# Kernel optimization log

Hardware: AMD Instinct MI355X
Metric: run time of the kernel (lower is better)

The kernel has to match this reference:

```python
import jax, jax.numpy as jnp
import numpy as np

N, E = 50000, 300000
IN, HID, OUT, HEADS = 768, 256, 128, 8
RELS = ("writes", "written_by", "cites")


def setup_inputs():
    ks = iter(jax.random.split(jax.random.key(0), 64))

    def nrm(shape, scale=1.0):
        return jax.random.normal(next(ks), shape, dtype=jnp.float32) * scale

    inp = {"x_paper": nrm((N, IN)), "x_author": nrm((N, IN))}
    for name in ("ei_writes", "ei_written_by", "ei_cites"):
        inp[name] = jax.random.randint(next(ks), (2, E), 0, N, dtype=jnp.int32)
    # layer 0: in=IN, out=HID, heads=HEADS
    s0 = 1.0 / np.sqrt(IN)
    inp["W0_paper"] = nrm((IN, HID), s0); inp["b0_paper"] = jnp.zeros((HID,), jnp.float32)
    inp["W0_author"] = nrm((IN, HID), s0); inp["b0_author"] = jnp.zeros((HID,), jnp.float32)
    D0 = HID // HEADS
    for rel in RELS:
        inp["a0s_" + rel] = nrm((HEADS, D0), 0.1)
        inp["a0d_" + rel] = nrm((HEADS, D0), 0.1)
    inp["Wk0"] = nrm((HID, HID), 1.0 / np.sqrt(HID)); inp["bk0"] = jnp.zeros((HID,), jnp.float32)
    inp["q0"] = nrm((HID,), 0.1)
    # layer 1 (last): in=HID, out=OUT, heads=1
    s1 = 1.0 / np.sqrt(HID)
    inp["W1_paper"] = nrm((HID, OUT), s1); inp["b1_paper"] = jnp.zeros((OUT,), jnp.float32)
    inp["W1_author"] = nrm((HID, OUT), s1); inp["b1_author"] = jnp.zeros((OUT,), jnp.float32)
    for rel in RELS:
        inp["a1s_" + rel] = nrm((1, OUT), 0.1)
        inp["a1d_" + rel] = nrm((1, OUT), 0.1)
    inp["Wk1"] = nrm((OUT, OUT), 1.0 / np.sqrt(OUT)); inp["bk1"] = jnp.zeros((OUT,), jnp.float32)
    inp["q1"] = nrm((OUT,), 0.1)
    return inp


def _han_layer(xs, proj, att, Wk, bk, q, edges, heads):
    # xs: {ntype: [N, in]}, proj: {ntype: (W, b)}, att: {rel: (a_src[H,D], a_dst[H,D])}
    C = q.shape[0]
    D = C // heads
    xh = {nt: (x @ proj[nt][0] + proj[nt][1]).reshape(-1, heads, D) for nt, x in xs.items()}
    outs = {nt: [] for nt in xs}
    for (st, rel, dt), ei in edges:
        a_s, a_d = att[rel]
        xsrc, xdst = xh[st], xh[dt]
        src, dst = ei[0], ei[1]
        n = xdst.shape[0]
        # GAT-style edge scores per head: [E, H]
        al = jax.nn.leaky_relu((xsrc * a_s).sum(-1)[src] + (xdst * a_d).sum(-1)[dst], 0.2)
        amax = jax.lax.stop_gradient(jax.ops.segment_max(al, dst, num_segments=n))
        ex = jnp.exp(al - amax[dst])
        alpha = ex / (jax.ops.segment_sum(ex, dst, num_segments=n)[dst] + 1e-16)
        msg = xsrc[src] * alpha[:, :, None]                      # [E, H, D]
        agg = jax.ops.segment_sum(msg, dst, num_segments=n)      # [n, H, D]
        outs[dt].append(jax.nn.relu(agg.reshape(n, C)))
    # semantic attention across metapaths (group)
    res = {}
    for nt, lst in outs.items():
        stk = jnp.stack(lst)                                     # [M, n, C]
        score = (q * jnp.tanh(stk @ Wk + bk).mean(axis=1)).sum(-1)
        w = jax.nn.softmax(score)                                # [M]
        res[nt] = jnp.einsum('m,mnc->nc', w, stk)
    return res


def reference(x_paper, x_author, W0_paper, b0_paper, W0_author, b0_author,
              a0s_writes, a0d_writes, a0s_written_by, a0d_written_by, a0s_cites, a0d_cites,
              Wk0, bk0, q0,
              W1_paper, b1_paper, W1_author, b1_author,
              a1s_writes, a1d_writes, a1s_written_by, a1d_written_by, a1s_cites, a1d_cites,
              Wk1, bk1, q1,
              ei_writes, ei_written_by, ei_cites):
    edges = [(("author", "writes", "paper"), ei_writes),
             (("paper", "written_by", "author"), ei_written_by),
             (("paper", "cites", "paper"), ei_cites)]
    h = _han_layer({"paper": x_paper, "author": x_author},
                   {"paper": (W0_paper, b0_paper), "author": (W0_author, b0_author)},
                   {"writes": (a0s_writes, a0d_writes),
                    "written_by": (a0s_written_by, a0d_written_by),
                    "cites": (a0s_cites, a0d_cites)},
                   Wk0, bk0, q0, edges, HEADS)
    h = {k: jax.nn.elu(v) for k, v in h.items()}
    h = _han_layer(h,
                   {"paper": (W1_paper, b1_paper), "author": (W1_author, b1_author)},
                   {"writes": (a1s_writes, a1d_writes),
                    "written_by": (a1s_written_by, a1d_written_by),
                    "cites": (a1s_cites, a1d_cites)},
                   Wk1, bk1, q1, edges, 1)

    def l2n(v):
        return v / jnp.maximum(jnp.linalg.norm(v, axis=1, keepdims=True), 1e-12)

    return (l2n(h["paper"]), l2n(h["author"]))
```

## Files before the change

### kernel.cpp

```cpp
#include <hip/hip_runtime.h>
#include <math.h>

#define NN 50000
#define NE 300000
#define DIN 768
#define DHID 256
#define DOUT 128
#define H0 8
#define D0 32

typedef __attribute__((ext_vector_type(8))) short bf16x8;
typedef __attribute__((ext_vector_type(8))) unsigned short u16x8;
typedef __attribute__((ext_vector_type(4))) float f32x4;

__device__ __forceinline__ unsigned short f2bf(float f) {
    unsigned u = __float_as_uint(f);
    unsigned r = (u + 0x7fffu + ((u >> 16) & 1u)) >> 16;
    return (unsigned short)r;
}
__device__ __forceinline__ float bf2f(unsigned short u) {
    return __uint_as_float(((unsigned)u) << 16);
}

__device__ __forceinline__ void gload16(const void* g, void* l) {
    __builtin_amdgcn_global_load_lds(
        (const __attribute__((address_space(1))) unsigned int*)g,
        (__attribute__((address_space(3))) unsigned int*)l, 16, 0, 0);
}

__global__ void convert_bf16_kernel(const float* __restrict__ in, unsigned short* __restrict__ out, int n8)
{
    int i = blockIdx.x * 256 + threadIdx.x;
    if (i >= n8) return;
    float4 a = ((const float4*)in)[i * 2];
    float4 b = ((const float4*)in)[i * 2 + 1];
    u16x8 o;
    o[0] = f2bf(a.x); o[1] = f2bf(a.y); o[2] = f2bf(a.z); o[3] = f2bf(a.w);
    o[4] = f2bf(b.x); o[5] = f2bf(b.y); o[6] = f2bf(b.z); o[7] = f2bf(b.w);
    ((u16x8*)out)[i] = o;
}

__global__ void transconv_kernel(const float* __restrict__ W, unsigned short* __restrict__ Wt,
                                 int K, int Nc)
{
    int gid = blockIdx.x * 256 + threadIdx.x;
    if (gid >= K * Nc) return;
    int k = gid / Nc, n = gid - k * Nc;
    Wt[(size_t)n * K + k] = f2bf(W[gid]);
}

__global__ __launch_bounds__(256) void gemm_bf16_kernel(
    const unsigned short* __restrict__ A0, const unsigned short* __restrict__ A1,
    const unsigned short* __restrict__ Bt0, const unsigned short* __restrict__ Bt1,
    const float* __restrict__ bias0, const float* __restrict__ bias1,
    unsigned short* __restrict__ C0, unsigned short* __restrict__ C1,
    int M, int K, int Nc)
{
    __shared__ __align__(16) unsigned short As[2][128 * 32];
    __shared__ __align__(16) unsigned short Bs[2][128 * 32];
    const int z = blockIdx.z;
    const unsigned short* A  = z ? A1  : A0;
    const unsigned short* Bt = z ? Bt1 : Bt0;
    const float* bias = z ? bias1 : bias0;
    unsigned short* C = z ? C1 : C0;
    const int t = threadIdx.x;
    const int lane = t & 63, w = t >> 6;
    const int wr = w >> 1, wc = w & 1;
    const int bm = blockIdx.y * 128, bn = blockIdx.x * 128;

    f32x4 acc[4][4];
    #pragma unroll
    for (int m = 0; m < 4; ++m)
        #pragma unroll
        for (int n = 0; n < 4; ++n)
            acc[m][n] = (f32x4){0.f, 0.f, 0.f, 0.f};

    const int c0 = w * 64 + lane, c1 = c0 + 256;
    const int row0 = c0 >> 2, row1 = c1 >> 2;
    const int g0 = (c0 & 3) ^ ((row0 >> 1) & 3);
    const int g1 = (c1 & 3) ^ ((row1 >> 1) & 3);
    const int ar0 = (bm + row0 < M) ? (bm + row0) : (M - 1);
    const int ar1 = (bm + row1 < M) ? (bm + row1) : (M - 1);
    const unsigned short* pA0 = A + (size_t)ar0 * K + g0 * 8;
    const unsigned short* pA1 = A + (size_t)ar1 * K + g1 * 8;
    const unsigned short* pB0 = Bt + (size_t)(bn + row0) * K + g0 * 8;
    const unsigned short* pB1 = Bt + (size_t)(bn + row1) * K + g1 * 8;

    const int rA = wr * 64 + (lane & 15);
    const int rB = wc * 64 + (lane & 15);
    const int gw = lane >> 4;
    const int nt = K >> 5;

    gload16(pA0, &As[0][c0 * 8]);
    gload16(pA1, &As[0][c1 * 8]);
    gload16(pB0, &Bs[0][c0 * 8]);
    gload16(pB1, &Bs[0][c1 * 8]);
    __syncthreads();
    for (int ti = 0; ti < nt; ++ti) {
        const int cur = ti & 1;
        if (ti + 1 < nt) {
            const int nk = (ti + 1) << 5;
            const int nb = cur ^ 1;
            gload16(pA0 + nk, &As[nb][c0 * 8]);
            gload16(pA1 + nk, &As[nb][c1 * 8]);
            gload16(pB0 + nk, &Bs[nb][c0 * 8]);
            gload16(pB1 + nk, &Bs[nb][c1 * 8]);
        }
        bf16x8 afr[4], bfr[4];
        #pragma unroll
        for (int m = 0; m < 4; ++m) {
            int r = rA + m * 16;
            afr[m] = *(const bf16x8*)&As[cur][r * 32 + ((gw ^ ((r >> 1) & 3)) * 8)];
        }
        #pragma unroll
        for (int n = 0; n < 4; ++n) {
            int r = rB + n * 16;
            bfr[n] = *(const bf16x8*)&Bs[cur][r * 32 + ((gw ^ ((r >> 1) & 3)) * 8)];
        }
        #pragma unroll
        for (int m = 0; m < 4; ++m)
            #pragma unroll
            for (int n = 0; n < 4; ++n)
                acc[m][n] = __builtin_amdgcn_mfma_f32_16x16x32_bf16(afr[m], bfr[n], acc[m][n], 0, 0, 0);
        __syncthreads();
    }
    #pragma unroll
    for (int m = 0; m < 4; ++m) {
        #pragma unroll
        for (int j = 0; j < 4; ++j) {
            int row = bm + wr * 64 + m * 16 + (lane >> 4) * 4 + j;
            if (row >= M) continue;
            #pragma unroll
            for (int n = 0; n < 4; ++n) {
                int col = bn + wc * 64 + n * 16 + (lane & 15);
                C[(size_t)row * Nc + col] = f2bf(acc[m][n][j] + bias[col]);
            }
        }
    }
}

__global__ __launch_bounds__(256) void sem_bf16_kernel(
    const unsigned short* __restrict__ A, const unsigned short* __restrict__ Bt,
    const float* __restrict__ bk, float* __restrict__ partial,
    int M, int K, int Nc)
{
    __shared__ __align__(16) unsigned short As[2][128 * 32];
    __shared__ __align__(16) unsigned short Bs[2][128 * 32];
    __shared__ float red[128];
    const int t = threadIdx.x;
    const int lane = t & 63, w = t >> 6;
    const int wr = w >> 1, wc = w & 1;
    const int bm = blockIdx.y * 128, bn = blockIdx.x * 128;

    f32x4 acc[4][4];
    #pragma unroll
    for (int m = 0; m < 4; ++m)
        #pragma unroll
        for (int n = 0; n < 4; ++n)
            acc[m][n] = (f32x4){0.f, 0.f, 0.f, 0.f};

    const int c0 = w * 64 + lane, c1 = c0 + 256;
    const int row0 = c0 >> 2, row1 = c1 >> 2;
    const int g0 = (c0 & 3) ^ ((row0 >> 1) & 3);
    const int g1 = (c1 & 3) ^ ((row1 >> 1) & 3);
    const int ar0 = (bm + row0 < M) ? (bm + row0) : (M - 1);
    const int ar1 = (bm + row1 < M) ? (bm + row1) : (M - 1);
    const unsigned short* pA0 = A + (size_t)ar0 * K + g0 * 8;
    const unsigned short* pA1 = A + (size_t)ar1 * K + g1 * 8;
    const unsigned short* pB0 = Bt + (size_t)(bn + row0) * K + g0 * 8;
    const unsigned short* pB1 = Bt + (size_t)(bn + row1) * K + g1 * 8;

    const int rA = wr * 64 + (lane & 15);
    const int rB = wc * 64 + (lane & 15);
    const int gw = lane >> 4;
    const int nt = K >> 5;

    gload16(pA0, &As[0][c0 * 8]);
    gload16(pA1, &As[0][c1 * 8]);
    gload16(pB0, &Bs[0][c0 * 8]);
    gload16(pB1, &Bs[0][c1 * 8]);
    __syncthreads();
    for (int ti = 0; ti < nt; ++ti) {
        const int cur = ti & 1;
        if (ti + 1 < nt) {
            const int nk = (ti + 1) << 5;
            const int nb = cur ^ 1;
            gload16(pA0 + nk, &As[nb][c0 * 8]);
            gload16(pA1 + nk, &As[nb][c1 * 8]);
            gload16(pB0 + nk, &Bs[nb][c0 * 8]);
            gload16(pB1 + nk, &Bs[nb][c1 * 8]);
        }
        bf16x8 afr[4], bfr[4];
        #pragma unroll
        for (int m = 0; m < 4; ++m) {
            int r = rA + m * 16;
            afr[m] = *(const bf16x8*)&As[cur][r * 32 + ((gw ^ ((r >> 1) & 3)) * 8)];
        }
        #pragma unroll
        for (int n = 0; n < 4; ++n) {
            int r = rB + n * 16;
            bfr[n] = *(const bf16x8*)&Bs[cur][r * 32 + ((gw ^ ((r >> 1) & 3)) * 8)];
        }
        #pragma unroll
        for (int m = 0; m < 4; ++m)
            #pragma unroll
            for (int n = 0; n < 4; ++n)
                acc[m][n] = __builtin_amdgcn_mfma_f32_16x16x32_bf16(afr[m], bfr[n], acc[m][n], 0, 0, 0);
        __syncthreads();
    }
    if (t < 128) red[t] = 0.f;
    __syncthreads();
    #pragma unroll
    for (int n = 0; n < 4; ++n) {
        int lcol = wc * 64 + n * 16 + (lane & 15);
        float b = bk[bn + lcol];
        float s = 0.f;
        #pragma unroll
        for (int m = 0; m < 4; ++m) {
            #pragma unroll
            for (int j = 0; j < 4; ++j) {
                int row = bm + wr * 64 + m * 16 + (lane >> 4) * 4 + j;
                if (row < M) s += tanhf(acc[m][n][j] + b);
            }
        }
        atomicAdd(&red[lcol], s);
    }
    __syncthreads();
    if (t < 128) atomicAdd(&partial[bn + t], red[t]);
}

__global__ void hist_kernel(const int* __restrict__ dst, int* __restrict__ deg, int E)
{
    int e = blockIdx.x * 256 + threadIdx.x;
    if (e < E) atomicAdd(&deg[dst[e]], 1);
}

__global__ void block_sum_kernel(const int* __restrict__ deg, int* __restrict__ bsum, int n)
{
    __shared__ int buf[256];
    int i = blockIdx.x * 256 + threadIdx.x;
    buf[threadIdx.x] = (i < n) ? deg[i] : 0;
    __syncthreads();
    for (int s = 128; s > 0; s >>= 1) {
        if (threadIdx.x < s) buf[threadIdx.x] += buf[threadIdx.x + s];
        __syncthreads();
    }
    if (threadIdx.x == 0) bsum[blockIdx.x] = buf[0];
}

__global__ void scan_bsum_kernel(const int* __restrict__ bsum, int* __restrict__ boff, int nb)
{
    __shared__ int buf[256];
    int tid = threadIdx.x;
    int v = (tid < nb) ? bsum[tid] : 0;
    buf[tid] = v;
    __syncthreads();
    for (int off = 1; off < 256; off <<= 1) {
        int t = (tid >= off) ? buf[tid - off] : 0;
        __syncthreads();
        buf[tid] += t;
        __syncthreads();
    }
    if (tid < nb) boff[tid] = buf[tid] - v;
}

__global__ void scan_final_kernel(const int* __restrict__ deg, const int* __restrict__ boff,
                                  int* __restrict__ offs, int n)
{
    __shared__ int buf[256];
    int tid = threadIdx.x, b = blockIdx.x;
    int i = b * 256 + tid;
    int v = (i < n) ? deg[i] : 0;
    buf[tid] = v;
    __syncthreads();
    for (int off = 1; off < 256; off <<= 1) {
        int t = (tid >= off) ? buf[tid - off] : 0;
        __syncthreads();
        buf[tid] += t;
        __syncthreads();
    }
    if (i < n) offs[i] = boff[b] + buf[tid] - v;
    if (i == n - 1) offs[n] = boff[b] + buf[tid];
}

__global__ void place_kernel(const int* __restrict__ src, const int* __restrict__ dst,
                             const int* __restrict__ offs, int* __restrict__ cnt,
                             int* __restrict__ esrc, int E)
{
    int e = blockIdx.x * 256 + threadIdx.x;
    if (e >= E) return;
    int d = dst[e];
    int p = offs[d] + atomicAdd(&cnt[d], 1);
    esrc[p] = src[e];
}

__global__ void scores_L0_kernel(
    const unsigned short* __restrict__ xp, const unsigned short* __restrict__ xa,
    const float* __restrict__ a_dw, const float* __restrict__ a_swb,
    const float* __restrict__ a_sc, const float* __restrict__ a_dc,
    const float* __restrict__ a_sw, const float* __restrict__ a_dwb,
    float* __restrict__ sW_dst, float* __restrict__ sWB_src,
    float* __restrict__ sC_src, float* __restrict__ sC_dst,
    float* __restrict__ sW_src, float* __restrict__ sWB_dst)
{
    int gid = blockIdx.x * 256 + threadIdx.x;
    int half = NN * H0;
    if (gid >= 2 * half) return;
    if (gid < half) {
        int node = gid >> 3, h = gid & 7;
        const unsigned short* xr = xp + (size_t)node * DHID + h * D0;
        float xv[D0];
        #pragma unroll
        for (int j = 0; j < 4; ++j) {
            u16x8 v = ((const u16x8*)xr)[j];
            #pragma unroll
            for (int k = 0; k < 8; ++k) xv[j * 8 + k] = bf2f(v[k]);
        }
        const float* p0 = a_dw  + h * D0;
        const float* p1 = a_swb + h * D0;
        const float* p2 = a_sc  + h * D0;
        const float* p3 = a_dc  + h * D0;
        float d0 = 0.f, d1 = 0.f, d2 = 0.f, d3 = 0.f;
        #pragma unroll
        for (int k = 0; k < D0; ++k) {
            float x = xv[k];
            d0 += x * p0[k]; d1 += x * p1[k]; d2 += x * p2[k]; d3 += x * p3[k];
        }
        sW_dst[gid] = d0; sWB_src[gid] = d1; sC_src[gid] = d2; sC_dst[gid] = d3;
    } else {
        int g = gid - half;
        int node = g >> 3, h = g & 7;
        const unsigned short* xr = xa + (size_t)node * DHID + h * D0;
        float xv[D0];
        #pragma unroll
        for (int j = 0; j < 4; ++j) {
            u16x8 v = ((const u16x8*)xr)[j];
            #pragma unroll
            for (int k = 0; k < 8; ++k) xv[j * 8 + k] = bf2f(v[k]);
        }
        const float* p0 = a_sw  + h * D0;
        const float* p1 = a_dwb + h * D0;
        float d0 = 0.f, d1 = 0.f;
        #pragma unroll
        for (int k = 0; k < D0; ++k) {
            float x = xv[k];
            d0 += x * p0[k]; d1 += x * p1[k];
        }
        sW_src[g] = d0; sWB_dst[g] = d1;
    }
}

__global__ void scores_L1_kernel(
    const unsigned short* __restrict__ xp, const unsigned short* __restrict__ xa,
    const float* __restrict__ a_dw, const float* __restrict__ a_swb,
    const float* __restrict__ a_sc, const float* __restrict__ a_dc,
    const float* __restrict__ a_sw, const float* __restrict__ a_dwb,
    float* __restrict__ sW_dst, float* __restrict__ sWB_src,
    float* __restrict__ sC_src, float* __restrict__ sC_dst,
    float* __restrict__ sW_src, float* __restrict__ sWB_dst)
{
    int gid = blockIdx.x * 256 + threadIdx.x;
    if (gid >= 2 * NN) return;
    if (gid < NN) {
        const unsigned short* xr = xp + (size_t)gid * DOUT;
        float d0 = 0.f, d1 = 0.f, d2 = 0.f, d3 = 0.f;
        for (int j = 0; j < DOUT / 8; ++j) {
            u16x8 v = ((const u16x8*)xr)[j];
            #pragma unroll
            for (int k = 0; k < 8; ++k) {
                float x = bf2f(v[k]);
                int c = j * 8 + k;
                d0 += x * a_dw[c]; d1 += x * a_swb[c]; d2 += x * a_sc[c]; d3 += x * a_dc[c];
            }
        }
        sW_dst[gid] = d0; sWB_src[gid] = d1; sC_src[gid] = d2; sC_dst[gid] = d3;
    } else {
        int g = gid - NN;
        const unsigned short* xr = xa + (size_t)g * DOUT;
        float d0 = 0.f, d1 = 0.f;
        for (int j = 0; j < DOUT / 8; ++j) {
            u16x8 v = ((const u16x8*)xr)[j];
            #pragma unroll
            for (int k = 0; k < 8; ++k) {
                float x = bf2f(v[k]);
                int c = j * 8 + k;
                d0 += x * a_sw[c]; d1 += x * a_dwb[c];
            }
        }
        sW_src[g] = d0; sWB_dst[g] = d1;
    }
}

__global__ void seg_alpha3_kernel(
    const int* __restrict__ of0, const int* __restrict__ of1, const int* __restrict__ of2,
    const int* __restrict__ es0, const int* __restrict__ es1, const int* __restrict__ es2,
    const float* __restrict__ ss0, const float* __restrict__ ss1, const float* __restrict__ ss2,
    const float* __restrict__ sd0, const float* __restrict__ sd1, const float* __restrict__ sd2,
    float* __restrict__ al0, float* __restrict__ al1, float* __restrict__ al2, int H)
{
    int rel = blockIdx.y;
    const int* offs = rel == 0 ? of0 : (rel == 1 ? of1 : of2);
    const int* esrc = rel == 0 ? es0 : (rel == 1 ? es1 : es2);
    const float* ssrc = rel == 0 ? ss0 : (rel == 1 ? ss1 : ss2);
    const float* sdst = rel == 0 ? sd0 : (rel == 1 ? sd1 : sd2);
    float* alpha = rel == 0 ? al0 : (rel == 1 ? al1 : al2);
    int gid = blockIdx.x * 256 + threadIdx.x;
    if (gid >= NN * H) return;
    int d = gid / H, h = gid - d * H;
    int beg = offs[d], end = offs[d + 1];
    float sd = sdst[gid];
    float m = -INFINITY, den = 0.f;
    for (int i = beg; i < end; ++i) {
        int s = esrc[i];
        float v = ssrc[s * H + h] + sd;
        v = (v >= 0.f) ? v : 0.2f * v;
        if (v > m) { den = den * expf(m - v) + 1.f; m = v; }
        else       den += expf(v - m);
    }
    float inv = 1.f / (den + 1e-16f);
    for (int i = beg; i < end; ++i) {
        int s = esrc[i];
        float v = ssrc[s * H + h] + sd;
        v = (v >= 0.f) ? v : 0.2f * v;
        alpha[(size_t)i * H + h] = expf(v - m) * inv;
    }
}

template<int CPL, int HH, int DSH>
__global__ __launch_bounds__(256) void gather3_kernel(
    const int* __restrict__ of0, const int* __restrict__ of1, const int* __restrict__ of2,
    const int* __restrict__ es0, const int* __restrict__ es1, const int* __restrict__ es2,
    const float* __restrict__ al0, const float* __restrict__ al1, const float* __restrict__ al2,
    const unsigned short* __restrict__ x0, const unsigned short* __restrict__ x1,
    const unsigned short* __restrict__ x2,
    unsigned short* __restrict__ o0, unsigned short* __restrict__ o1,
    unsigned short* __restrict__ o2, int C)
{
    int rel = blockIdx.y;
    const int* offs = rel == 0 ? of0 : (rel == 1 ? of1 : of2);
    const int* esrc = rel == 0 ? es0 : (rel == 1 ? es1 : es2);
    const float* alpha = rel == 0 ? al0 : (rel == 1 ? al1 : al2);
    const unsigned short* x = rel == 0 ? x0 : (rel == 1 ? x1 : x2);
    unsigned short* outp = rel == 0 ? o0 : (rel == 1 ? o1 : o2);

    int wid = threadIdx.x >> 6, lane = threadIdx.x & 63;
    int d = blockIdx.x * 4 + wid;
    int c0 = lane * CPL;
    int h = c0 >> DSH;
    int beg = offs[d], end = offs[d + 1];
    float acc[CPL];
    #pragma unroll
    for (int j = 0; j < CPL; ++j) acc[j] = 0.f;
    for (int i = beg; i < end; ++i) {
        int s = esrc[i];
        float a = alpha[(size_t)i * HH + h];
        const unsigned short* xp = x + (size_t)s * C + c0;
        if (CPL == 4) {
            ushort4 xv = *(const ushort4*)xp;
            acc[0] += a * bf2f(xv.x); acc[1] += a * bf2f(xv.y);
            acc[2] += a * bf2f(xv.z); acc[3] += a * bf2f(xv.w);
        } else {
            ushort2 xv = *(const ushort2*)xp;
            acc[0] += a * bf2f(xv.x); acc[1] += a * bf2f(xv.y);
        }
    }
    unsigned short* op = outp + (size_t)d * C + c0;
    if (CPL == 4) {
        ushort4 st;
        st.x = f2bf(fmaxf(acc[0], 0.f)); st.y = f2bf(fmaxf(acc[1], 0.f));
        st.z = f2bf(fmaxf(acc[2], 0.f)); st.w = f2bf(fmaxf(acc[3], 0.f));
        *(ushort4*)op = st;
    } else {
        ushort2 st;
        st.x = f2bf(fmaxf(acc[0], 0.f)); st.y = f2bf(fmaxf(acc[1], 0.f));
        *(ushort2*)op = st;
    }
}

__global__ void sem_weights_kernel(const float* __restrict__ partial, const float* __restrict__ q,
                                   float* __restrict__ w, int C, int n)
{
    if (threadIdx.x != 0 || blockIdx.x != 0) return;
    float inv = 1.f / (float)n;
    float s0 = 0.f, s1 = 0.f;
    for (int c = 0; c < C; ++c) {
        s0 += q[c] * partial[c] * inv;
        s1 += q[c] * partial[C + c] * inv;
    }
    float m = fmaxf(s0, s1);
    float e0 = expf(s0 - m), e1 = expf(s1 - m);
    float den = e0 + e1;
    w[0] = e0 / den;
    w[1] = e1 / den;
}

__global__ void combine2_bf16_kernel(const unsigned short* __restrict__ a,
                                     const unsigned short* __restrict__ b,
                                     const float* __restrict__ w, unsigned short* __restrict__ out,
                                     int n8)
{
    int i = blockIdx.x * 256 + threadIdx.x;
    if (i >= n8) return;
    float w0 = w[0], w1 = w[1];
    u16x8 va = ((const u16x8*)a)[i];
    u16x8 vb = ((const u16x8*)b)[i];
    u16x8 o;
    #pragma unroll
    for (int j = 0; j < 8; ++j) o[j] = f2bf(w0 * bf2f(va[j]) + w1 * bf2f(vb[j]));
    ((u16x8*)out)[i] = o;
}

__global__ __launch_bounds__(128) void final_norm_kernel(
    const unsigned short* __restrict__ aggW, const unsigned short* __restrict__ aggC,
    const unsigned short* __restrict__ aggB, const float* __restrict__ w,
    float* __restrict__ out)
{
    __shared__ float red[128];
    int row = blockIdx.x;
    int c = threadIdx.x;
    float v;
    if (row < NN) {
        size_t i = (size_t)row * DOUT + c;
        v = w[0] * bf2f(aggW[i]) + w[1] * bf2f(aggC[i]);
    } else {
        size_t i = (size_t)(row - NN) * DOUT + c;
        v = bf2f(aggB[i]);
    }
    red[c] = v * v;
    __syncthreads();
    for (int s = 64; s > 0; s >>= 1) {
        if (c < s) red[c] += red[c + s];
        __syncthreads();
    }
    float norm = sqrtf(red[0]);
    out[(size_t)row * DOUT + c] = v / fmaxf(norm, 1e-12f);
}

static void build_csr(const int* ei, int* offs, int* esrc, int* deg, int* bsum, int* boff,
                      hipStream_t stream)
{
    const int* src = ei;
    const int* dst = ei + NE;
    const int NB = (NN + 255) / 256;
    hipMemsetAsync(deg, 0, NN * sizeof(int), stream);
    hist_kernel<<<(NE + 255) / 256, 256, 0, stream>>>(dst, deg, NE);
    block_sum_kernel<<<NB, 256, 0, stream>>>(deg, bsum, NN);
    scan_bsum_kernel<<<1, 256, 0, stream>>>(bsum, boff, NB);
    scan_final_kernel<<<NB, 256, 0, stream>>>(deg, boff, offs, NN);
    hipMemsetAsync(deg, 0, NN * sizeof(int), stream);
    place_kernel<<<(NE + 255) / 256, 256, 0, stream>>>(src, dst, offs, deg, esrc, NE);
}

extern "C" void kernel_launch(void* const* d_in, const int* in_sizes, int n_in,
                              void* d_out, int out_size, void* d_ws, size_t ws_size,
                              hipStream_t stream)
{
    const float* x_paper   = (const float*)d_in[0];
    const float* x_author  = (const float*)d_in[1];
    const int*   ei_writes = (const int*)d_in[2];
    const int*   ei_wb     = (const int*)d_in[3];
    const int*   ei_cites  = (const int*)d_in[4];
    const float* W0p = (const float*)d_in[5];  const float* b0p = (const float*)d_in[6];
    const float* W0a = (const float*)d_in[7];  const float* b0a = (const float*)d_in[8];
    const float* a0s_w  = (const float*)d_in[9];  const float* a0d_w  = (const float*)d_in[10];
    const float* a0s_wb = (const float*)d_in[11]; const float* a0d_wb = (const float*)d_in[12];
    const float* a0s_c  = (const float*)d_in[13]; const float* a0d_c  = (const float*)d_in[14];
    const float* Wk0 = (const float*)d_in[15]; const float* bk0 = (const float*)d_in[16];
    const float* q0  = (const float*)d_in[17];
    const float* W1p = (const float*)d_in[18]; const float* b1p = (const float*)d_in[19];
    const float* W1a = (const float*)d_in[20]; const float* b1a = (const float*)d_in[21];
    const float* a1s_w  = (const float*)d_in[22]; const float* a1d_w  = (const float*)d_in[23];
    const float* a1s_wb = (const float*)d_in[24]; const float* a1d_wb = (const float*)d_in[25];
    const float* a1s_c  = (const float*)d_in[26]; const float* a1d_c  = (const float*)d_in[27];
    const float* Wk1 = (const float*)d_in[28]; const float* bk1 = (const float*)d_in[29];
    const float* q1  = (const float*)d_in[30];

    float* out = (float*)d_out;

    const size_t NH = (size_t)NN * DHID;
    const size_t NI = (size_t)NN * DIN;
    const size_t NO = (size_t)NN * DOUT;
    const size_t NH2 = NH * 2;
    const size_t NI2 = NI * 2;
    const size_t NO2 = NO * 2;

    char* base = (char*)d_ws;
    unsigned short* xbhP = (unsigned short*)(base + 0);
    unsigned short* xbhA = (unsigned short*)(base + NH2);
    unsigned short* xbP  = (unsigned short*)(base + 2 * NH2);
    unsigned short* xbA  = (unsigned short*)(base + 2 * NH2 + NI2);
    unsigned short* aggW = (unsigned short*)(base + 2 * NH2);
    unsigned short* aggC = (unsigned short*)(base + 3 * NH2);
    unsigned short* aggB = (unsigned short*)(base + 4 * NH2);
    unsigned short* hbP  = (unsigned short*)(base + 0);
    unsigned short* hbA  = aggB;
    unsigned short* x1Pb = (unsigned short*)(base + NH2);
    unsigned short* x1Ab = (unsigned short*)(base + NH2 + NO2);
    unsigned short* agg1W = (unsigned short*)(base + 2 * NH2 + NI2);
    unsigned short* agg1C = (unsigned short*)(base + 2 * NH2 + NI2 + NO2);
    unsigned short* agg1B = (unsigned short*)(base + 2 * NH2 + NI2 + 2 * NO2);
    float* sW_src  = (float*)(base + 204800000);
    float* sW_dst  = sW_src  + NN * H0;
    float* sWB_src = sW_dst  + NN * H0;
    float* sWB_dst = sWB_src + NN * H0;
    float* sC_src  = sWB_dst + NN * H0;
    float* sC_dst  = sC_src  + NN * H0;
    float* al0 = (float*)(base + 214400000);
    float* al1 = al0 + (size_t)NE * H0;
    float* al2 = al1 + (size_t)NE * H0;
    int* ip      = (int*)(base + 243200000);
    int* offsW   = ip;               ip += NN + 4;
    int* offsWB  = ip;               ip += NN + 4;
    int* offsC   = ip;               ip += NN + 4;
    int* esrcW   = ip;               ip += NE;
    int* esrcWB  = ip;               ip += NE;
    int* esrcC   = ip;               ip += NE;
    int* deg     = ip;               ip += NN;
    int* bsum    = ip;               ip += 256;
    int* boff    = ip;               ip += 256;
    unsigned short* wt0p = (unsigned short*)ip;
    unsigned short* wt0a = wt0p + (size_t)DHID * DIN;
    unsigned short* wkt  = wt0a + (size_t)DHID * DIN;
    unsigned short* wt1p = wt0p;
    unsigned short* wt1a = wt1p + (size_t)DOUT * DHID;
    float* tsum = (float*)(wkt + (size_t)DHID * DHID);
    float* wsem = tsum + 512;

    build_csr(ei_writes, offsW,  esrcW,  deg, bsum, boff, stream);
    build_csr(ei_wb,     offsWB, esrcWB, deg, bsum, boff, stream);
    build_csr(ei_cites,  offsC,  esrcC,  deg, bsum, boff, stream);

    hipMemsetAsync(tsum, 0, 512 * sizeof(float), stream);
    convert_bf16_kernel<<<(int)((NI / 8 + 255) / 256), 256, 0, stream>>>(x_paper,  xbP, (int)(NI / 8));
    convert_bf16_kernel<<<(int)((NI / 8 + 255) / 256), 256, 0, stream>>>(x_author, xbA, (int)(NI / 8));
    transconv_kernel<<<(DIN * DHID + 255) / 256, 256, 0, stream>>>(W0p, wt0p, DIN, DHID);
    transconv_kernel<<<(DIN * DHID + 255) / 256, 256, 0, stream>>>(W0a, wt0a, DIN, DHID);
    transconv_kernel<<<(DHID * DHID + 255) / 256, 256, 0, stream>>>(Wk0, wkt, DHID, DHID);

    dim3 g0(DHID / 128, (NN + 127) / 128, 2);
    gemm_bf16_kernel<<<g0, 256, 0, stream>>>(xbP, xbA, wt0p, wt0a, b0p, b0a, xbhP, xbhA, NN, DIN, DHID);

    scores_L0_kernel<<<(2 * NN * H0 + 255) / 256, 256, 0, stream>>>(
        xbhP, xbhA, a0d_w, a0s_wb, a0s_c, a0d_c, a0s_w, a0d_wb,
        sW_dst, sWB_src, sC_src, sC_dst, sW_src, sWB_dst);
    dim3 ga0((NN * H0 + 255) / 256, 3);
    seg_alpha3_kernel<<<ga0, 256, 0, stream>>>(
        offsW, offsWB, offsC, esrcW, esrcWB, esrcC,
        sW_src, sWB_src, sC_src, sW_dst, sWB_dst, sC_dst, al0, al1, al2, H0);
    dim3 gg0(NN / 4, 3);
    gather3_kernel<4, H0, 5><<<gg0, 256, 0, stream>>>(
        offsW, offsWB, offsC, esrcW, esrcWB, esrcC, al0, al1, al2,
        xbhA, xbhP, xbhP, aggW, aggB, aggC, DHID);

    dim3 gs0(DHID / 128, (NN + 127) / 128);
    sem_bf16_kernel<<<gs0, 256, 0, stream>>>(aggW, wkt, bk0, tsum,        NN, DHID, DHID);
    sem_bf16_kernel<<<gs0, 256, 0, stream>>>(aggC, wkt, bk0, tsum + DHID, NN, DHID, DHID);
    sem_weights_kernel<<<1, 64, 0, stream>>>(tsum, q0, wsem, DHID, NN);

    combine2_bf16_kernel<<<(int)((NH / 8 + 255) / 256), 256, 0, stream>>>(aggW, aggC, wsem, hbP, (int)(NH / 8));

    transconv_kernel<<<(DHID * DOUT + 255) / 256, 256, 0, stream>>>(W1p, wt1p, DHID, DOUT);
    transconv_kernel<<<(DHID * DOUT + 255) / 256, 256, 0, stream>>>(W1a, wt1a, DHID, DOUT);
    transconv_kernel<<<(DOUT * DOUT + 255) / 256, 256, 0, stream>>>(Wk1, wkt, DOUT, DOUT);

    dim3 g1(DOUT / 128, (NN + 127) / 128, 2);
    gemm_bf16_kernel<<<g1, 256, 0, stream>>>(hbP, hbA, wt1p, wt1a, b1p, b1a, x1Pb, x1Ab, NN, DHID, DOUT);

    hipMemsetAsync(tsum, 0, 2 * DOUT * sizeof(float), stream);

    scores_L1_kernel<<<(2 * NN + 255) / 256, 256, 0, stream>>>(
        x1Pb, x1Ab, a1d_w, a1s_wb, a1s_c, a1d_c, a1s_w, a1d_wb,
        sW_dst, sWB_src, sC_src, sC_dst, sW_src, sWB_dst);
    dim3 ga1((NN + 255) / 256, 3);
    seg_alpha3_kernel<<<ga1, 256, 0, stream>>>(
        offsW, offsWB, offsC, esrcW, esrcWB, esrcC,
        sW_src, sWB_src, sC_src, sW_dst, sWB_dst, sC_dst, al0, al1, al2, 1);
    dim3 gg1(NN / 4, 3);
    gather3_kernel<2, 1, 7><<<gg1, 256, 0, stream>>>(
        offsW, offsWB, offsC, esrcW, esrcWB, esrcC, al0, al1, al2,
        x1Ab, x1Pb, x1Pb, agg1W, agg1B, agg1C, DOUT);

    dim3 gs1(DOUT / 128, (NN + 127) / 128);
    sem_bf16_kernel<<<gs1, 256, 0, stream>>>(agg1W, wkt, bk1, tsum,        NN, DOUT, DOUT);
    sem_bf16_kernel<<<gs1, 256, 0, stream>>>(agg1C, wkt, bk1, tsum + DOUT, NN, DOUT, DOUT);
    sem_weights_kernel<<<1, 64, 0, stream>>>(tsum, q1, wsem, DOUT, NN);

    final_norm_kernel<<<2 * NN, 128, 0, stream>>>(agg1W, agg1C, agg1B, wsem, out);
}
```

Measured before the change: 871.8 us.

## Batch CSR build and weight conversions across relations, prefetch in gather

```diff
diff --git a/kernel.cpp b/kernel.cpp
--- a/kernel.cpp
+++ b/kernel.cpp
@@ -8,6 +8,7 @@
 #define DOUT 128
 #define H0 8
 #define D0 32
+#define OFFST (NN + 4)
 
 typedef __attribute__((ext_vector_type(8))) short bf16x8;
 typedef __attribute__((ext_vector_type(8))) unsigned short u16x8;
@@ -28,10 +29,15 @@
         (__attribute__((address_space(3))) unsigned int*)l, 16, 0, 0);
 }
 
-__global__ void convert_bf16_kernel(const float* __restrict__ in, unsigned short* __restrict__ out, int n8)
-{
-    int i = blockIdx.x * 256 + threadIdx.x;
-    if (i >= n8) return;
+__global__ void convert2_bf16_kernel(const float* __restrict__ in0, const float* __restrict__ in1,
+                                     unsigned short* __restrict__ o0, unsigned short* __restrict__ o1,
+                                     int n8)
+{
+    int gid = blockIdx.x * 256 + threadIdx.x;
+    if (gid >= 2 * n8) return;
+    const float* in = (gid < n8) ? in0 : in1;
+    unsigned short* out = (gid < n8) ? o0 : o1;
+    int i = (gid < n8) ? gid : gid - n8;
     float4 a = ((const float4*)in)[i * 2];
     float4 b = ((const float4*)in)[i * 2 + 1];
     u16x8 o;
@@ -40,13 +46,21 @@
     ((u16x8*)out)[i] = o;
 }
 
-__global__ void transconv_kernel(const float* __restrict__ W, unsigned short* __restrict__ Wt,
-                                 int K, int Nc)
-{
+__global__ void transconv3_kernel(const float* __restrict__ Wa, const float* __restrict__ Wb,
+                                  const float* __restrict__ Wc,
+                                  unsigned short* __restrict__ Ta, unsigned short* __restrict__ Tb,
+                                  unsigned short* __restrict__ Tc,
+                                  int Kab, int Nab, int Kc, int Ncc)
+{
+    int y = blockIdx.y;
+    const float* W = (y == 0) ? Wa : ((y == 1) ? Wb : Wc);
+    unsigned short* T = (y == 0) ? Ta : ((y == 1) ? Tb : Tc);
+    int K = (y == 2) ? Kc : Kab;
+    int Nc = (y == 2) ? Ncc : Nab;
     int gid = blockIdx.x * 256 + threadIdx.x;
     if (gid >= K * Nc) return;
     int k = gid / Nc, n = gid - k * Nc;
-    Wt[(size_t)n * K + k] = f2bf(W[gid]);
+    T[(size_t)n * K + k] = f2bf(W[gid]);
 }
 
 __global__ __launch_bounds__(256) void gemm_bf16_kernel(
@@ -229,30 +243,36 @@
     if (t < 128) atomicAdd(&partial[bn + t], red[t]);
 }
 
-__global__ void hist_kernel(const int* __restrict__ dst, int* __restrict__ deg, int E)
-{
-    int e = blockIdx.x * 256 + threadIdx.x;
-    if (e < E) atomicAdd(&deg[dst[e]], 1);
-}
-
-__global__ void block_sum_kernel(const int* __restrict__ deg, int* __restrict__ bsum, int n)
+__global__ void hist3_kernel(const int* __restrict__ d0, const int* __restrict__ d1,
+                             const int* __restrict__ d2, int* __restrict__ deg3)
+{
+    int gid = blockIdx.x * 256 + threadIdx.x;
+    if (gid >= 3 * NE) return;
+    int rel = gid / NE, e = gid - rel * NE;
+    const int* dst = (rel == 0) ? d0 : ((rel == 1) ? d1 : d2);
+    atomicAdd(&deg3[rel * NN + dst[e]], 1);
+}
+
+__global__ void block_sum3_kernel(const int* __restrict__ deg3, int* __restrict__ bsum3)
 {
     __shared__ int buf[256];
+    int rel = blockIdx.y;
     int i = blockIdx.x * 256 + threadIdx.x;
-    buf[threadIdx.x] = (i < n) ? deg[i] : 0;
+    buf[threadIdx.x] = (i < NN) ? deg3[rel * NN + i] : 0;
     __syncthreads();
     for (int s = 128; s > 0; s >>= 1) {
         if (threadIdx.x < s) buf[threadIdx.x] += buf[threadIdx.x + s];
         __syncthreads();
     }
-    if (threadIdx.x == 0) bsum[blockIdx.x] = buf[0];
-}
-
-__global__ void scan_bsum_kernel(const int* __restrict__ bsum, int* __restrict__ boff, int nb)
+    if (threadIdx.x == 0) bsum3[rel * 256 + blockIdx.x] = buf[0];
+}
+
+__global__ void scan_bsum3_kernel(const int* __restrict__ bsum3, int* __restrict__ boff3, int nb)
 {
     __shared__ int buf[256];
+    int rel = blockIdx.y;
     int tid = threadIdx.x;
-    int v = (tid < nb) ? bsum[tid] : 0;
+    int v = (tid < nb) ? bsum3[rel * 256 + tid] : 0;
     buf[tid] = v;
     __syncthreads();
     for (int off = 1; off < 256; off <<= 1) {
@@ -261,16 +281,17 @@
         buf[tid] += t;
         __syncthreads();
     }
-    if (tid < nb) boff[tid] = buf[tid] - v;
-}
-
-__global__ void scan_final_kernel(const int* __restrict__ deg, const int* __restrict__ boff,
-                                  int* __restrict__ offs, int n)
+    if (tid < nb) boff3[rel * 256 + tid] = buf[tid] - v;
+}
+
+__global__ void scan_final3_kernel(const int* __restrict__ deg3, const int* __restrict__ boff3,
+                                   int* __restrict__ offs3)
 {
     __shared__ int buf[256];
+    int rel = blockIdx.y;
     int tid = threadIdx.x, b = blockIdx.x;
     int i = b * 256 + tid;
-    int v = (i < n) ? deg[i] : 0;
+    int v = (i < NN) ? deg3[rel * NN + i] : 0;
     buf[tid] = v;
     __syncthreads();
     for (int off = 1; off < 256; off <<= 1) {
@@ -279,19 +300,24 @@
         buf[tid] += t;
         __syncthreads();
     }
-    if (i < n) offs[i] = boff[b] + buf[tid] - v;
-    if (i == n - 1) offs[n] = boff[b] + buf[tid];
-}
-
-__global__ void place_kernel(const int* __restrict__ src, const int* __restrict__ dst,
-                             const int* __restrict__ offs, int* __restrict__ cnt,
-                             int* __restrict__ esrc, int E)
-{
+    int* offs = offs3 + rel * OFFST;
+    if (i < NN) offs[i] = boff3[rel * 256 + b] + buf[tid] - v;
+    if (i == NN - 1) offs[NN] = boff3[rel * 256 + b] + buf[tid];
+}
+
+__global__ void place3_kernel(const int* __restrict__ s0, const int* __restrict__ s1,
+                              const int* __restrict__ s2,
+                              const int* __restrict__ offs3, int* __restrict__ cnt3,
+                              int* __restrict__ esrc3)
+{
+    int rel = blockIdx.y;
     int e = blockIdx.x * 256 + threadIdx.x;
-    if (e >= E) return;
-    int d = dst[e];
-    int p = offs[d] + atomicAdd(&cnt[d], 1);
-    esrc[p] = src[e];
+    if (e >= NE) return;
+    const int* srcdst = (rel == 0) ? s0 : ((rel == 1) ? s1 : s2);
+    int src = srcdst[e];
+    int d = srcdst[NE + e];
+    int p = offs3[rel * OFFST + d] + atomicAdd(&cnt3[rel * NN + d], 1);
+    esrc3[rel * NE + p] = src;
 }
 
 __global__ void scores_L0_kernel(
@@ -392,18 +418,17 @@
 }
 
 __global__ void seg_alpha3_kernel(
-    const int* __restrict__ of0, const int* __restrict__ of1, const int* __restrict__ of2,
-    const int* __restrict__ es0, const int* __restrict__ es1, const int* __restrict__ es2,
+    const int* __restrict__ offs3, const int* __restrict__ esrc3,
     const float* __restrict__ ss0, const float* __restrict__ ss1, const float* __restrict__ ss2,
     const float* __restrict__ sd0, const float* __restrict__ sd1, const float* __restrict__ sd2,
-    float* __restrict__ al0, float* __restrict__ al1, float* __restrict__ al2, int H)
+    float* __restrict__ alpha3, int H)
 {
     int rel = blockIdx.y;
-    const int* offs = rel == 0 ? of0 : (rel == 1 ? of1 : of2);
-    const int* esrc = rel == 0 ? es0 : (rel == 1 ? es1 : es2);
-    const float* ssrc = rel == 0 ? ss0 : (rel == 1 ? ss1 : ss2);
-    const float* sdst = rel == 0 ? sd0 : (rel == 1 ? sd1 : sd2);
-    float* alpha = rel == 0 ? al0 : (rel == 1 ? al1 : al2);
+    const int* offs = offs3 + rel * OFFST;
+    const int* esrc = esrc3 + rel * NE;
+    const float* ssrc = (rel == 0) ? ss0 : ((rel == 1) ? ss1 : ss2);
+    const float* sdst = (rel == 0) ? sd0 : ((rel == 1) ? sd1 : sd2);
+    float* alpha = alpha3 + (size_t)rel * NE * H0;
     int gid = blockIdx.x * 256 + threadIdx.x;
     if (gid >= NN * H) return;
     int d = gid / H, h = gid - d * H;
@@ -428,51 +453,64 @@
 
 template<int CPL, int HH, int DSH>
 __global__ __launch_bounds__(256) void gather3_kernel(
-    const int* __restrict__ of0, const int* __restrict__ of1, const int* __restrict__ of2,
-    const int* __restrict__ es0, const int* __restrict__ es1, const int* __restrict__ es2,
-    const float* __restrict__ al0, const float* __restrict__ al1, const float* __restrict__ al2,
+    const int* __restrict__ offs3, const int* __restrict__ esrc3,
+    const float* __restrict__ alpha3,
     const unsigned short* __restrict__ x0, const unsigned short* __restrict__ x1,
     const unsigned short* __restrict__ x2,
     unsigned short* __restrict__ o0, unsigned short* __restrict__ o1,
     unsigned short* __restrict__ o2, int C)
 {
     int rel = blockIdx.y;
-    const int* offs = rel == 0 ? of0 : (rel == 1 ? of1 : of2);
-    const int* esrc = rel == 0 ? es0 : (rel == 1 ? es1 : es2);
-    const float* alpha = rel == 0 ? al0 : (rel == 1 ? al1 : al2);
-    const unsigned short* x = rel == 0 ? x0 : (rel == 1 ? x1 : x2);
-    unsigned short* outp = rel == 0 ? o0 : (rel == 1 ? o1 : o2);
+    const int* offs = offs3 + rel * OFFST;
+    const int* esrc = esrc3 + rel * NE;
+    const float* alpha = alpha3 + (size_t)rel * NE * H0;
+    const unsigned short* x = (rel == 0) ? x0 : ((rel == 1) ? x1 : x2);
+    unsigned short* outp = (rel == 0) ? o0 : ((rel == 1) ? o1 : o2);
 
     int wid = threadIdx.x >> 6, lane = threadIdx.x & 63;
     int d = blockIdx.x * 4 + wid;
     int c0 = lane * CPL;
     int h = c0 >> DSH;
     int beg = offs[d], end = offs[d + 1];
-    float acc[CPL];
-    #pragma unroll
-    for (int j = 0; j < CPL; ++j) acc[j] = 0.f;
-    for (int i = beg; i < end; ++i) {
-        int s = esrc[i];
-        float a = alpha[(size_t)i * HH + h];
-        const unsigned short* xp = x + (size_t)s * C + c0;
+    float acc0 = 0.f, acc1 = 0.f, acc2 = 0.f, acc3 = 0.f;
+    int n = end - beg;
+    if (n > 0) {
+        int sA = esrc[beg];
+        float aA = alpha[(size_t)beg * HH + h];
+        int sB = sA; float aB = 0.f;
+        if (n > 1) { sB = esrc[beg + 1]; aB = alpha[(size_t)(beg + 1) * HH + h]; }
         if (CPL == 4) {
-            ushort4 xv = *(const ushort4*)xp;
-            acc[0] += a * bf2f(xv.x); acc[1] += a * bf2f(xv.y);
-            acc[2] += a * bf2f(xv.z); acc[3] += a * bf2f(xv.w);
+            ushort4 xc = *(const ushort4*)(x + (size_t)sA * C + c0);
+            for (int i = beg; i < end; ++i) {
+                ushort4 xn = xc;
+                if (i + 1 < end) xn = *(const ushort4*)(x + (size_t)sB * C + c0);
+                int sN = sB; float aN = 0.f;
+                if (i + 2 < end) { sN = esrc[i + 2]; aN = alpha[(size_t)(i + 2) * HH + h]; }
+                acc0 += aA * bf2f(xc.x); acc1 += aA * bf2f(xc.y);
+                acc2 += aA * bf2f(xc.z); acc3 += aA * bf2f(xc.w);
+                xc = xn; aA = aB; sB = sN; aB = aN;
+            }
         } else {
-            ushort2 xv = *(const ushort2*)xp;
-            acc[0] += a * bf2f(xv.x); acc[1] += a * bf2f(xv.y);
+            ushort2 xc = *(const ushort2*)(x + (size_t)sA * C + c0);
+            for (int i = beg; i < end; ++i) {
+                ushort2 xn = xc;
+                if (i + 1 < end) xn = *(const ushort2*)(x + (size_t)sB * C + c0);
+                int sN = sB; float aN = 0.f;
+                if (i + 2 < end) { sN = esrc[i + 2]; aN = alpha[(size_t)(i + 2) * HH + h]; }
+                acc0 += aA * bf2f(xc.x); acc1 += aA * bf2f(xc.y);
+                xc = xn; aA = aB; sB = sN; aB = aN;
+            }
         }
     }
     unsigned short* op = outp + (size_t)d * C + c0;
     if (CPL == 4) {
         ushort4 st;
-        st.x = f2bf(fmaxf(acc[0], 0.f)); st.y = f2bf(fmaxf(acc[1], 0.f));
-        st.z = f2bf(fmaxf(acc[2], 0.f)); st.w = f2bf(fmaxf(acc[3], 0.f));
+        st.x = f2bf(fmaxf(acc0, 0.f)); st.y = f2bf(fmaxf(acc1, 0.f));
+        st.z = f2bf(fmaxf(acc2, 0.f)); st.w = f2bf(fmaxf(acc3, 0.f));
         *(ushort4*)op = st;
     } else {
         ushort2 st;
-        st.x = f2bf(fmaxf(acc[0], 0.f)); st.y = f2bf(fmaxf(acc[1], 0.f));
+        st.x = f2bf(fmaxf(acc0, 0.f)); st.y = f2bf(fmaxf(acc1, 0.f));
         *(ushort2*)op = st;
     }
 }
@@ -534,21 +572,6 @@
     }
     float norm = sqrtf(red[0]);
     out[(size_t)row * DOUT + c] = v / fmaxf(norm, 1e-12f);
-}
-
-static void build_csr(const int* ei, int* offs, int* esrc, int* deg, int* bsum, int* boff,
-                      hipStream_t stream)
-{
-    const int* src = ei;
-    const int* dst = ei + NE;
-    const int NB = (NN + 255) / 256;
-    hipMemsetAsync(deg, 0, NN * sizeof(int), stream);
-    hist_kernel<<<(NE + 255) / 256, 256, 0, stream>>>(dst, deg, NE);
-    block_sum_kernel<<<NB, 256, 0, stream>>>(deg, bsum, NN);
-    scan_bsum_kernel<<<1, 256, 0, stream>>>(bsum, boff, NB);
-    scan_final_kernel<<<NB, 256, 0, stream>>>(deg, boff, offs, NN);
-    hipMemsetAsync(deg, 0, NN * sizeof(int), stream);
-    place_kernel<<<(NE + 255) / 256, 256, 0, stream>>>(src, dst, offs, deg, esrc, NE);
 }
 
 extern "C" void kernel_launch(void* const* d_in, const int* in_sizes, int n_in,
@@ -599,25 +622,20 @@
     unsigned short* agg1W = (unsigned short*)(base + 2 * NH2 + NI2);
     unsigned short* agg1C = (unsigned short*)(base + 2 * NH2 + NI2 + NO2);
     unsigned short* agg1B = (unsigned short*)(base + 2 * NH2 + NI2 + 2 * NO2);
+
     float* sW_src  = (float*)(base + 204800000);
     float* sW_dst  = sW_src  + NN * H0;
     float* sWB_src = sW_dst  + NN * H0;
     float* sWB_dst = sWB_src + NN * H0;
     float* sC_src  = sWB_dst + NN * H0;
     float* sC_dst  = sC_src  + NN * H0;
-    float* al0 = (float*)(base + 214400000);
-    float* al1 = al0 + (size_t)NE * H0;
-    float* al2 = al1 + (size_t)NE * H0;
-    int* ip      = (int*)(base + 243200000);
-    int* offsW   = ip;               ip += NN + 4;
-    int* offsWB  = ip;               ip += NN + 4;
-    int* offsC   = ip;               ip += NN + 4;
-    int* esrcW   = ip;               ip += NE;
-    int* esrcWB  = ip;               ip += NE;
-    int* esrcC   = ip;               ip += NE;
-    int* deg     = ip;               ip += NN;
-    int* bsum    = ip;               ip += 256;
-    int* boff    = ip;               ip += 256;
+    float* alpha3  = (float*)(base + 214400000);
+    int* ip     = (int*)(base + 243200000);
+    int* offs3  = ip;  ip += 3 * OFFST;
+    int* esrc3  = ip;  ip += 3 * NE;
+    int* deg3   = ip;  ip += 3 * NN;
+    int* bsum3  = ip;  ip += 3 * 256;
+    int* boff3  = ip;  ip += 3 * 256;
     unsigned short* wt0p = (unsigned short*)ip;
     unsigned short* wt0a = wt0p + (size_t)DHID * DIN;
     unsigned short* wkt  = wt0a + (size_t)DHID * DIN;
@@ -626,16 +644,20 @@
     float* tsum = (float*)(wkt + (size_t)DHID * DHID);
     float* wsem = tsum + 512;
 
-    build_csr(ei_writes, offsW,  esrcW,  deg, bsum, boff, stream);
-    build_csr(ei_wb,     offsWB, esrcWB, deg, bsum, boff, stream);
-    build_csr(ei_cites,  offsC,  esrcC,  deg, bsum, boff, stream);
+    const int NB = (NN + 255) / 256;
+
+    hipMemsetAsync(deg3, 0, 3 * NN * sizeof(int), stream);
+    hist3_kernel<<<(3 * NE + 255) / 256, 256, 0, stream>>>(ei_writes + NE, ei_wb + NE, ei_cites + NE, deg3);
+    block_sum3_kernel<<<dim3(NB, 3), 256, 0, stream>>>(deg3, bsum3);
+    scan_bsum3_kernel<<<dim3(1, 3), 256, 0, stream>>>(bsum3, boff3, NB);
+    scan_final3_kernel<<<dim3(NB, 3), 256, 0, stream>>>(deg3, boff3, offs3);
+    hipMemsetAsync(deg3, 0, 3 * NN * sizeof(int), stream);
+    place3_kernel<<<dim3((NE + 255) / 256, 3), 256, 0, stream>>>(ei_writes, ei_wb, ei_cites, offs3, deg3, esrc3);
 
     hipMemsetAsync(tsum, 0, 512 * sizeof(float), stream);
-    convert_bf16_kernel<<<(int)((NI / 8 + 255) / 256), 256, 0, stream>>>(x_paper,  xbP, (int)(NI / 8));
-    convert_bf16_kernel<<<(int)((NI / 8 + 255) / 256), 256, 0, stream>>>(x_author, xbA, (int)(NI / 8));
-    transconv_kernel<<<(DIN * DHID + 255) / 256, 256, 0, stream>>>(W0p, wt0p, DIN, DHID);
-    transconv_kernel<<<(DIN * DHID + 255) / 256, 256, 0, stream>>>(W0a, wt0a, DIN, DHID);
-    transconv_kernel<<<(DHID * DHID + 255) / 256, 256, 0, stream>>>(Wk0, wkt, DHID, DHID);
+    convert2_bf16_kernel<<<(int)((2 * NI / 8 + 255) / 256), 256, 0, stream>>>(x_paper, x_author, xbP, xbA, (int)(NI / 8));
+    transconv3_kernel<<<dim3((DIN * DHID + 255) / 256, 3), 256, 0, stream>>>(
+        W0p, W0a, Wk0, wt0p, wt0a, wkt, DIN, DHID, DHID, DHID);
 
     dim3 g0(DHID / 128, (NN + 127) / 128, 2);
     gemm_bf16_kernel<<<g0, 256, 0, stream>>>(xbP, xbA, wt0p, wt0a, b0p, b0a, xbhP, xbhA, NN, DIN, DHID);
@@ -645,12 +667,10 @@
         sW_dst, sWB_src, sC_src, sC_dst, sW_src, sWB_dst);
     dim3 ga0((NN * H0 + 255) / 256, 3);
     seg_alpha3_kernel<<<ga0, 256, 0, stream>>>(
-        offsW, offsWB, offsC, esrcW, esrcWB, esrcC,
-        sW_src, sWB_src, sC_src, sW_dst, sWB_dst, sC_dst, al0, al1, al2, H0);
+        offs3, esrc3, sW_src, sWB_src, sC_src, sW_dst, sWB_dst, sC_dst, alpha3, H0);
     dim3 gg0(NN / 4, 3);
     gather3_kernel<4, H0, 5><<<gg0, 256, 0, stream>>>(
-        offsW, offsWB, offsC, esrcW, esrcWB, esrcC, al0, al1, al2,
-        xbhA, xbhP, xbhP, aggW, aggB, aggC, DHID);
+        offs3, esrc3, alpha3, xbhA, xbhP, xbhP, aggW, aggB, aggC, DHID);
 
     dim3 gs0(DHID / 128, (NN + 127) / 128);
     sem_bf16_kernel<<<gs0, 256, 0, stream>>>(aggW, wkt, bk0, tsum,        NN, DHID, DHID);
@@ -659,9 +679,8 @@
 
     combine2_bf16_kernel<<<(int)((NH / 8 + 255) / 256), 256, 0, stream>>>(aggW, aggC, wsem, hbP, (int)(NH / 8));
 
-    transconv_kernel<<<(DHID * DOUT + 255) / 256, 256, 0, stream>>>(W1p, wt1p, DHID, DOUT);
-    transconv_kernel<<<(DHID * DOUT + 255) / 256, 256, 0, stream>>>(W1a, wt1a, DHID, DOUT);
-    transconv_kernel<<<(DOUT * DOUT + 255) / 256, 256, 0, stream>>>(Wk1, wkt, DOUT, DOUT);
+    transconv3_kernel<<<dim3((DHID * DOUT + 255) / 256, 3), 256, 0, stream>>>(
+        W1p, W1a, Wk1, wt1p, wt1a, wkt, DHID, DOUT, DOUT, DOUT);
 
     dim3 g1(DOUT / 128, (NN + 127) / 128, 2);
     gemm_bf16_kernel<<<g1, 256, 0, stream>>>(hbP, hbA, wt1p, wt1a, b1p, b1a, x1Pb, x1Ab, NN, DHID, DOUT);
@@ -673,12 +692,10 @@
         sW_dst, sWB_src, sC_src, sC_dst, sW_src, sWB_dst);
     dim3 ga1((NN + 255) / 256, 3);
     seg_alpha3_kernel<<<ga1, 256, 0, stream>>>(
-        offsW, offsWB, offsC, esrcW, esrcWB, esrcC,
-        sW_src, sWB_src, sC_src, sW_dst, sWB_dst, sC_dst, al0, al1, al2, 1);
+        offs3, esrc3, sW_src, sWB_src, sC_src, sW_dst, sWB_dst, sC_dst, alpha3, 1);
     dim3 gg1(NN / 4, 3);
     gather3_kernel<2, 1, 7><<<gg1, 256, 0, stream>>>(
-        offsW, offsWB, offsC, esrcW, esrcWB, esrcC, al0, al1, al2,
-        x1Ab, x1Pb, x1Pb, agg1W, agg1B, agg1C, DOUT);
+        offs3, esrc3, alpha3, x1Ab, x1Pb, x1Pb, agg1W, agg1B, agg1C, DOUT);
 
     dim3 gs1(DOUT / 128, (NN + 127) / 128);
     sem_bf16_kernel<<<gs1, 256, 0, stream>>>(agg1W, wkt, bk1, tsum,        NN, DOUT, DOUT);
```

Measured after the change: 779.5 us. -10.6%, faster.
